# Optimization experiments

Measured on AMD Instinct MI355X. Metric: run time of the kernel, lower is better.

Reference implementation:

```python
import jax, jax.numpy as jnp
import numpy as np

N = 50000
E = 800000
D_IN = 128
D_OUT = 128
BN_EPS = 1e-5


def setup_inputs() -> dict:
    key = jax.random.key(0)
    ks = jax.random.split(key, 9)
    feature = jax.random.normal(ks[0], (N, D_IN), dtype=jnp.float32)
    snorm_n = jax.random.uniform(ks[1], (N, 1), dtype=jnp.float32)
    edge_src = jax.random.randint(ks[2], (E,), 0, N, dtype=jnp.int32)
    edge_dst = jax.random.randint(ks[3], (E,), 0, N, dtype=jnp.int32)
    # Linear(in,out,bias=False) weights, applied as x @ W (W stored [in,out])
    s = 1.0 / np.sqrt(D_IN)
    W1 = jax.random.uniform(ks[4], (D_IN, D_OUT), jnp.float32, -s, s)
    W2 = jax.random.uniform(ks[5], (D_IN, D_OUT), jnp.float32, -s, s)
    W3 = jax.random.uniform(ks[6], (D_IN, D_OUT), jnp.float32, -s, s)
    bias = jnp.zeros((D_OUT,), jnp.float32)
    gamma = jnp.ones((D_OUT,), jnp.float32)
    beta = jnp.zeros((D_OUT,), jnp.float32)
    return {"feature": feature, "snorm_n": snorm_n, "W1": W1, "W2": W2,
            "W3": W3, "bias": bias, "gamma": gamma, "beta": beta,
            "edge_src": edge_src, "edge_dst": edge_dst}


def _mpconv(feat, norm, edge_src, edge_dst):
    # feat: [N, D]; norm: [N, 1] = clamp(in_deg,1)^-0.5
    h = feat * norm
    msg = h[edge_src]                                   # gather [E, D]
    agg = jax.ops.segment_sum(msg, edge_dst, num_segments=N)  # scatter-add
    return agg * norm


def reference(feature, snorm_n, W1, W2, W3, bias, gamma, beta,
              edge_src, edge_dst):
    # in-degree normalization (same graph for both MP passes)
    deg = jax.ops.segment_sum(jnp.ones_like(edge_dst, jnp.float32),
                              edge_dst, num_segments=N)
    norm = jnp.power(jnp.clip(deg, 1.0, None), -0.5)[:, None]  # [N,1]

    h_in = feature
    ax = _mpconv(feature, norm, edge_src, edge_dst)
    ax2 = _mpconv(ax, norm, edge_src, edge_dst)

    h = (feature @ W1) + ((-ax) @ W2) + ((2.0 * ax2 - feature) @ W3) + bias
    h = h * snorm_n  # graph_norm

    # BatchNorm1d over nodes (training-mode batch statistics, biased var)
    mean = jnp.mean(h, axis=0)
    var = jnp.mean(jnp.square(h - mean), axis=0)
    h = (h - mean) * jax.lax.rsqrt(var + BN_EPS) * gamma + beta

    h = jax.nn.relu(h)      # activation
    h = h_in + h            # residual (in_dim == out_dim)
    # dropout p=0.0 -> identity
    return h
```

## Files before the change

kernel.cpp:

```cpp
#include <hip/hip_runtime.h>
#include <hip/hip_bf16.h>

#define NN 50000
#define NE 800000
#define DD 128
#define BN_EPS 1e-5f
#define SCAN_G 98

typedef unsigned short ushort_t;
typedef unsigned int uint_t;
typedef __attribute__((ext_vector_type(8))) short short8v;
typedef __attribute__((ext_vector_type(4))) float f32x4;

__device__ __forceinline__ float b2f(ushort_t u) {
    union { uint_t i; float f; } v; v.i = ((uint_t)u) << 16; return v.f;
}
__device__ __forceinline__ ushort_t f2b(float f) {
    uint_t u = __float_as_uint(f);
    u += 0x7FFFu + ((u >> 16) & 1u);
    return (ushort_t)(u >> 16);
}
__device__ __forceinline__ void atomAdd(float* p, float v) { unsafeAtomicAdd(p, v); }

__global__ void epos_kernel(const int* __restrict__ dst, int* __restrict__ cnt,
                            int* __restrict__ epos) {
    int e = blockIdx.x * 256 + threadIdx.x;
    if (e < NE) epos[e] = atomicAdd(&cnt[dst[e]], 1);
}

__global__ __launch_bounds__(512) void scan_part(const int* __restrict__ deg,
                                                 int* __restrict__ part,
                                                 float* __restrict__ norm) {
    int i = blockIdx.x * 512 + threadIdx.x;
    int v = (i < NN) ? deg[i] : 0;
    if (i < NN) norm[i] = rsqrtf((float)max(v, 1));
    int s = v;
    #pragma unroll
    for (int k = 1; k < 64; k <<= 1) s += __shfl_xor(s, k);
    __shared__ int wsum[8];
    if ((threadIdx.x & 63) == 0) wsum[threadIdx.x >> 6] = s;
    __syncthreads();
    if (threadIdx.x == 0) {
        int t = 0;
        #pragma unroll
        for (int k = 0; k < 8; ++k) t += wsum[k];
        part[blockIdx.x] = t;
    }
}

__global__ __launch_bounds__(512) void scan_final(const int* __restrict__ deg,
                                                  const int* __restrict__ part,
                                                  int* __restrict__ off) {
    __shared__ int wsum[8];
    __shared__ int sbase;
    int t = threadIdx.x;
    int lane = t & 63, wv = t >> 6;

    int p = (t < blockIdx.x && t < SCAN_G) ? part[t] : 0;
    #pragma unroll
    for (int s = 1; s < 64; s <<= 1) p += __shfl_xor(p, s);
    if (lane == 0) wsum[wv] = p;
    __syncthreads();
    if (t == 0) {
        int b = 0;
        #pragma unroll
        for (int k = 0; k < 8; ++k) b += wsum[k];
        sbase = b;
    }
    __syncthreads();

    int i = blockIdx.x * 512 + t;
    int v = (i < NN) ? deg[i] : 0;
    int incl = v;
    #pragma unroll
    for (int s = 1; s < 64; s <<= 1) {
        int u = __shfl_up(incl, s);
        if (lane >= s) incl += u;
    }
    __syncthreads();
    if (lane == 63) wsum[wv] = incl;
    __syncthreads();
    int woff = 0;
    for (int k = 0; k < wv; ++k) woff += wsum[k];
    int excl = sbase + woff + incl - v;
    if (i < NN) off[i] = excl;
    if (blockIdx.x == 0 && t == 0) off[NN] = NE;
}

__global__ void fill_kernel(const int* __restrict__ src, const int* __restrict__ dst,
                            const int* __restrict__ epos, const int* __restrict__ off,
                            const float* __restrict__ norm, int2* __restrict__ csr) {
    int e = blockIdx.x * 256 + threadIdx.x;
    if (e >= NE) return;
    int s = src[e];
    int p = off[dst[e]] + epos[e];
    csr[p] = make_int2(s, __float_as_int(norm[s]));
}

__global__ void prep_kernel(const float* __restrict__ feat, ushort_t* __restrict__ feat_bf,
                            const float* __restrict__ W1, const float* __restrict__ W2,
                            const float* __restrict__ W3, ushort_t* __restrict__ wcT) {
    int b = blockIdx.x;
    if (b < 6250) {
        int i = b * 256 + threadIdx.x;
        float4 v = reinterpret_cast<const float4*>(feat)[i];
        ushort4 o = { f2b(v.x), f2b(v.y), f2b(v.z), f2b(v.w) };
        reinterpret_cast<ushort4*>(feat_bf)[i] = o;
    } else {
        int i = (b - 6250) * 256 + threadIdx.x;
        if (i >= DD * 384) return;
        int d = i / 384, k = i % 384;
        float v;
        if (k < 128)      v = W1[k * DD + d] - W3[k * DD + d];
        else if (k < 256) v = -W2[(k - 128) * DD + d];
        else              v = 2.0f * W3[(k - 256) * DD + d];
        wcT[i] = f2b(v);
    }
}

__global__ __launch_bounds__(256) void gather_bf(const ushort_t* __restrict__ x,
                                                 const float* __restrict__ norm,
                                                 const int* __restrict__ off,
                                                 const int2* __restrict__ csr,
                                                 ushort_t* __restrict__ out) {
    int wid = (blockIdx.x << 2) + (threadIdx.x >> 6);
    int lane = threadIdx.x & 63;
    int q = lane >> 4, l4 = lane & 15;
    int jb = off[wid], je = off[wid + 1];
    const uint4* xp = reinterpret_cast<const uint4*>(x);
    float a0 = 0.f, a1 = 0.f, a2 = 0.f, a3 = 0.f;
    float a4 = 0.f, a5 = 0.f, a6 = 0.f, a7 = 0.f;

#define ACC(cc, vv)                                                  \
    {                                                                \
        float n_ = __int_as_float(cc.y);                             \
        a0 = fmaf(n_, b2f((ushort_t)vv.x), a0);                      \
        a1 = fmaf(n_, b2f((ushort_t)(vv.x >> 16)), a1);              \
        a2 = fmaf(n_, b2f((ushort_t)vv.y), a2);                      \
        a3 = fmaf(n_, b2f((ushort_t)(vv.y >> 16)), a3);              \
        a4 = fmaf(n_, b2f((ushort_t)vv.z), a4);                      \
        a5 = fmaf(n_, b2f((ushort_t)(vv.z >> 16)), a5);              \
        a6 = fmaf(n_, b2f((ushort_t)vv.w), a6);                      \
        a7 = fmaf(n_, b2f((ushort_t)(vv.w >> 16)), a7);              \
    }

    int j = jb;
    for (; j + 16 <= je; j += 16) {
        int2 c0 = csr[j + q];
        int2 c1 = csr[j + 4 + q];
        int2 c2 = csr[j + 8 + q];
        int2 c3 = csr[j + 12 + q];
        uint4 v0 = xp[(size_t)c0.x * 16 + l4];
        uint4 v1 = xp[(size_t)c1.x * 16 + l4];
        uint4 v2 = xp[(size_t)c2.x * 16 + l4];
        uint4 v3 = xp[(size_t)c3.x * 16 + l4];
        ACC(c0, v0); ACC(c1, v1); ACC(c2, v2); ACC(c3, v3);
    }
    for (; j < je; j += 4) {
        int jj = j + q;
        int2 c = (jj < je) ? csr[jj] : make_int2(0, 0);
        uint4 v = xp[(size_t)c.x * 16 + l4];
        ACC(c, v);
    }
#undef ACC

    a0 += __shfl_xor(a0, 16); a0 += __shfl_xor(a0, 32);
    a1 += __shfl_xor(a1, 16); a1 += __shfl_xor(a1, 32);
    a2 += __shfl_xor(a2, 16); a2 += __shfl_xor(a2, 32);
    a3 += __shfl_xor(a3, 16); a3 += __shfl_xor(a3, 32);
    a4 += __shfl_xor(a4, 16); a4 += __shfl_xor(a4, 32);
    a5 += __shfl_xor(a5, 16); a5 += __shfl_xor(a5, 32);
    a6 += __shfl_xor(a6, 16); a6 += __shfl_xor(a6, 32);
    a7 += __shfl_xor(a7, 16); a7 += __shfl_xor(a7, 32);
    if (q == 0) {
        float nd = norm[wid];
        uint4 o;
        o.x = (uint_t)f2b(nd * a0) | ((uint_t)f2b(nd * a1) << 16);
        o.y = (uint_t)f2b(nd * a2) | ((uint_t)f2b(nd * a3) << 16);
        o.z = (uint_t)f2b(nd * a4) | ((uint_t)f2b(nd * a5) << 16);
        o.w = (uint_t)f2b(nd * a6) | ((uint_t)f2b(nd * a7) << 16);
        reinterpret_cast<uint4*>(out)[(size_t)wid * 16 + l4] = o;
    }
}

__global__ __launch_bounds__(256) void gemm_bn(
    const ushort_t* __restrict__ feat_bf, const ushort_t* __restrict__ ax_bf,
    const ushort_t* __restrict__ ax2_bf, const ushort_t* __restrict__ wcT,
    const float* __restrict__ bias, const float* __restrict__ snorm,
    ushort_t* __restrict__ t_out, float* __restrict__ gsums, float* __restrict__ gsq)
{
    __shared__ ushort_t As[128 * 128];
    __shared__ ushort_t Bs[128 * 128];
    int tid = threadIdx.x;
    int w = tid >> 6, lane = tid & 63;
    int row0 = blockIdx.x * 128;

    f32x4 acc[2][8] = {};

    #pragma unroll
    for (int kt = 0; kt < 3; ++kt) {
        const ushort_t* S = (kt == 0) ? feat_bf : (kt == 1) ? ax_bf : ax2_bf;
        __syncthreads();
        {
            int r = tid >> 1, hh = tid & 1;
            int grow = min(row0 + r, NN - 1);
            const char* gsrc = (const char*)(S + grow * DD);
            char* dbase = (char*)As + r * 256;
            int sw = (r & 7) << 4;
            #pragma unroll
            for (int c = 0; c < 8; ++c) {
                int cb = hh * 128 + c * 16;
                *(short8v*)(dbase + (cb ^ sw)) = *(const short8v*)(gsrc + cb);
            }
        }
        {
            int cidx = tid >> 1, hh = tid & 1;
            const char* gsrc = (const char*)(wcT + cidx * 384 + kt * 128);
            char* dbase = (char*)Bs + cidx * 256;
            int sw = (cidx & 7) << 4;
            #pragma unroll
            for (int c = 0; c < 8; ++c) {
                int cb = hh * 128 + c * 16;
                *(short8v*)(dbase + (cb ^ sw)) = *(const short8v*)(gsrc + cb);
            }
        }
        __syncthreads();
        int l15 = lane & 15;
        int r0a = w * 32 + l15;
        int r1a = r0a + 16;
        #pragma unroll
        for (int ks = 0; ks < 4; ++ks) {
            int kb = ks * 64 + ((lane >> 4) << 4);
            short8v a0 = *(const short8v*)((const char*)As + r0a * 256 + (kb ^ ((r0a & 7) << 4)));
            short8v a1 = *(const short8v*)((const char*)As + r1a * 256 + (kb ^ ((r1a & 7) << 4)));
            #pragma unroll
            for (int cf = 0; cf < 8; ++cf) {
                int col = cf * 16 + l15;
                short8v b = *(const short8v*)((const char*)Bs + col * 256 + (kb ^ ((col & 7) << 4)));
                acc[0][cf] = __builtin_amdgcn_mfma_f32_16x16x32_bf16(a0, b, acc[0][cf], 0, 0, 0);
                acc[1][cf] = __builtin_amdgcn_mfma_f32_16x16x32_bf16(a1, b, acc[1][cf], 0, 0, 0);
            }
        }
    }

    int q = lane >> 4, c0 = lane & 15;
    float s1[8], s2[8];
    #pragma unroll
    for (int cf = 0; cf < 8; ++cf) { s1[cf] = 0.f; s2[cf] = 0.f; }

    #pragma unroll
    for (int g = 0; g < 2; ++g) {
        int rbase = row0 + w * 32 + g * 16 + q * 4;
        float sn[4];
        #pragma unroll
        for (int i = 0; i < 4; ++i) sn[i] = (rbase + i < NN) ? snorm[rbase + i] : 0.f;
        #pragma unroll
        for (int cf = 0; cf < 8; ++cf) {
            int col = cf * 16 + c0;
            float bc = bias[col];
            #pragma unroll
            for (int i = 0; i < 4; ++i) {
                int row = rbase + i;
                if (row < NN) {
                    float t = (acc[g][cf][i] + bc) * sn[i];
                    t_out[row * DD + col] = f2b(t);
                    s1[cf] += t; s2[cf] += t * t;
                }
            }
        }
    }
    #pragma unroll
    for (int cf = 0; cf < 8; ++cf) {
        s1[cf] += __shfl_xor(s1[cf], 16); s1[cf] += __shfl_xor(s1[cf], 32);
        s2[cf] += __shfl_xor(s2[cf], 16); s2[cf] += __shfl_xor(s2[cf], 32);
    }
    if (q == 0) {
        int slot = (blockIdx.x & 31) * DD;
        #pragma unroll
        for (int cf = 0; cf < 8; ++cf) {
            atomAdd(&gsums[slot + cf * 16 + c0], s1[cf]);
            atomAdd(&gsq[slot + cf * 16 + c0], s2[cf]);
        }
    }
}

__global__ void bn_finalize(const float* __restrict__ gsums, const float* __restrict__ gsq,
                            const float* __restrict__ gamma,
                            const float* __restrict__ beta,
                            float* __restrict__ scale, float* __restrict__ shift) {
    int d = threadIdx.x;
    float s1 = 0.f, s2 = 0.f;
    for (int c = 0; c < 32; ++c) { s1 += gsums[c * DD + d]; s2 += gsq[c * DD + d]; }
    float mean = s1 / (float)NN;
    float var  = s2 / (float)NN - mean * mean;
    float sc = gamma[d] * rsqrtf(var + BN_EPS);
    scale[d] = sc;
    shift[d] = beta[d] - mean * sc;
}

__global__ void epilogue(const ushort_t* __restrict__ t, const ushort_t* __restrict__ featb,
                         const float* __restrict__ scale, const float* __restrict__ shift,
                         float* __restrict__ out) {
    int i = blockIdx.x * 256 + threadIdx.x;
    if (i >= NN * DD / 4) return;
    int d0 = (i << 2) & 127;
    ushort4 tv = reinterpret_cast<const ushort4*>(t)[i];
    ushort4 fv = reinterpret_cast<const ushort4*>(featb)[i];
    float4 o;
    o.x = b2f(fv.x) + fmaxf(b2f(tv.x) * scale[d0 + 0] + shift[d0 + 0], 0.f);
    o.y = b2f(fv.y) + fmaxf(b2f(tv.y) * scale[d0 + 1] + shift[d0 + 1], 0.f);
    o.z = b2f(fv.z) + fmaxf(b2f(tv.z) * scale[d0 + 2] + shift[d0 + 2], 0.f);
    o.w = b2f(fv.w) + fmaxf(b2f(tv.w) * scale[d0 + 3] + shift[d0 + 3], 0.f);
    reinterpret_cast<float4*>(out)[i] = o;
}

extern "C" void kernel_launch(void* const* d_in, const int* in_sizes, int n_in,
                              void* d_out, int out_size, void* d_ws, size_t ws_size,
                              hipStream_t stream) {
    const float* feat  = (const float*)d_in[0];
    const float* snorm = (const float*)d_in[1];
    const float* W1    = (const float*)d_in[2];
    const float* W2    = (const float*)d_in[3];
    const float* W3    = (const float*)d_in[4];
    const float* bias  = (const float*)d_in[5];
    const float* gamma = (const float*)d_in[6];
    const float* beta  = (const float*)d_in[7];
    const int* esrc = (const int*)d_in[8];
    const int* edst = (const int*)d_in[9];
    float* out = (float*)d_out;

    char* ws = (char*)d_ws;
    ushort_t* t_bf    = (ushort_t*)(ws);
    int*      epos    = (int*)     (ws);
    ushort_t* feat_bf = (ushort_t*)(ws + 12800000);
    ushort_t* ax_bf   = (ushort_t*)(ws + 25600000);
    ushort_t* ax2_bf  = (ushort_t*)(ws + 38400000);
    int2*     csr     = (int2*)    (ws + 51200000);
    float*    norm    = (float*)   (ws + 57600000);
    int*      cnt     = (int*)     (ws + 57800000);
    float*    gsums   = (float*)   (ws + 58000000);
    float*    gsq     = (float*)   (ws + 58016384);
    int*      off     = (int*)     (ws + 58032768);
    int*      part    = (int*)     (ws + 58232832);
    float*    scale   = (float*)   (ws + 58233856);
    float*    shift   = (float*)   (ws + 58234368);
    ushort_t* wcT     = (ushort_t*)(ws + 58234880);

    hipMemsetAsync(ws + 57800000, 0, 232768, stream);

    epos_kernel<<<3125, 256, 0, stream>>>(edst, cnt, epos);
    scan_part  <<<SCAN_G, 512, 0, stream>>>(cnt, part, norm);
    scan_final <<<SCAN_G, 512, 0, stream>>>(cnt, part, off);
    fill_kernel<<<3125, 256, 0, stream>>>(esrc, edst, epos, off, norm, csr);

    prep_kernel<<<6442, 256, 0, stream>>>(feat, feat_bf, W1, W2, W3, wcT);

    gather_bf<<<12500, 256, 0, stream>>>(feat_bf, norm, off, csr, ax_bf);
    gather_bf<<<12500, 256, 0, stream>>>(ax_bf,   norm, off, csr, ax2_bf);

    gemm_bn<<<391, 256, 0, stream>>>(feat_bf, ax_bf, ax2_bf, wcT, bias, snorm,
                                     t_bf, gsums, gsq);
    bn_finalize<<<1, 128, 0, stream>>>(gsums, gsq, gamma, beta, scale, shift);
    epilogue   <<<6250, 256, 0, stream>>>(t_bf, feat_bf, scale, shift, out);
}
```

Baseline: 175.6 us.

## Map one 16-lane group per node in gather and fold prep into setup kernels

The gather kernel now gives each destination node a 16-lane group instead of a full 64-lane wavefront. Each lane loops over that node's edges serially, which removes the cross-lane shuffle reduction and the idle-quarter masking, and the kernel launches with a quarter as many blocks. The feature bf16 conversion moves into the epos kernel and the weight combine into extra blocks of scan_final, which drops the separate prep launch. The trade-off is fewer edge loads in flight per node and more divergence between the four nodes that share a wavefront when their degrees differ.

```diff
diff --git a/kernel.cpp b/kernel.cpp
--- a/kernel.cpp
+++ b/kernel.cpp
@@ -22,10 +22,20 @@
 }
 __device__ __forceinline__ void atomAdd(float* p, float v) { unsafeAtomicAdd(p, v); }
 
-__global__ void epos_kernel(const int* __restrict__ dst, int* __restrict__ cnt,
-                            int* __restrict__ epos) {
+__global__ void epos_prep(const int* __restrict__ dst, int* __restrict__ cnt,
+                          int* __restrict__ epos,
+                          const float* __restrict__ feat, ushort_t* __restrict__ feat_bf) {
     int e = blockIdx.x * 256 + threadIdx.x;
-    if (e < NE) epos[e] = atomicAdd(&cnt[dst[e]], 1);
+    {
+        const float4* fp = reinterpret_cast<const float4*>(feat);
+        ushort4* op = reinterpret_cast<ushort4*>(feat_bf);
+        int i = e << 1;
+        float4 v0 = fp[i], v1 = fp[i + 1];
+        ushort4 o0 = { f2b(v0.x), f2b(v0.y), f2b(v0.z), f2b(v0.w) };
+        ushort4 o1 = { f2b(v1.x), f2b(v1.y), f2b(v1.z), f2b(v1.w) };
+        op[i] = o0; op[i + 1] = o1;
+    }
+    epos[e] = atomicAdd(&cnt[dst[e]], 1);
 }
 
 __global__ __launch_bounds__(512) void scan_part(const int* __restrict__ deg,
@@ -50,7 +60,21 @@
 
 __global__ __launch_bounds__(512) void scan_final(const int* __restrict__ deg,
                                                   const int* __restrict__ part,
-                                                  int* __restrict__ off) {
+                                                  int* __restrict__ off,
+                                                  const float* __restrict__ W1,
+                                                  const float* __restrict__ W2,
+                                                  const float* __restrict__ W3,
+                                                  ushort_t* __restrict__ wcT) {
+    if (blockIdx.x >= SCAN_G) {
+        int i = (blockIdx.x - SCAN_G) * 512 + threadIdx.x;
+        int d = i / 384, k = i % 384;
+        float v;
+        if (k < 128)      v = W1[k * DD + d] - W3[k * DD + d];
+        else if (k < 256) v = -W2[(k - 128) * DD + d];
+        else              v = 2.0f * W3[(k - 256) * DD + d];
+        wcT[i] = f2b(v);
+        return;
+    }
     __shared__ int wsum[8];
     __shared__ int sbase;
     int t = threadIdx.x;
@@ -97,36 +121,14 @@
     csr[p] = make_int2(s, __float_as_int(norm[s]));
 }
 
-__global__ void prep_kernel(const float* __restrict__ feat, ushort_t* __restrict__ feat_bf,
-                            const float* __restrict__ W1, const float* __restrict__ W2,
-                            const float* __restrict__ W3, ushort_t* __restrict__ wcT) {
-    int b = blockIdx.x;
-    if (b < 6250) {
-        int i = b * 256 + threadIdx.x;
-        float4 v = reinterpret_cast<const float4*>(feat)[i];
-        ushort4 o = { f2b(v.x), f2b(v.y), f2b(v.z), f2b(v.w) };
-        reinterpret_cast<ushort4*>(feat_bf)[i] = o;
-    } else {
-        int i = (b - 6250) * 256 + threadIdx.x;
-        if (i >= DD * 384) return;
-        int d = i / 384, k = i % 384;
-        float v;
-        if (k < 128)      v = W1[k * DD + d] - W3[k * DD + d];
-        else if (k < 256) v = -W2[(k - 128) * DD + d];
-        else              v = 2.0f * W3[(k - 256) * DD + d];
-        wcT[i] = f2b(v);
-    }
-}
-
 __global__ __launch_bounds__(256) void gather_bf(const ushort_t* __restrict__ x,
                                                  const float* __restrict__ norm,
                                                  const int* __restrict__ off,
                                                  const int2* __restrict__ csr,
                                                  ushort_t* __restrict__ out) {
-    int wid = (blockIdx.x << 2) + (threadIdx.x >> 6);
-    int lane = threadIdx.x & 63;
-    int q = lane >> 4, l4 = lane & 15;
-    int jb = off[wid], je = off[wid + 1];
+    int g = (blockIdx.x << 4) | (threadIdx.x >> 4);
+    int l4 = threadIdx.x & 15;
+    int jb = off[g], je = off[g + 1];
     const uint4* xp = reinterpret_cast<const uint4*>(x);
     float a0 = 0.f, a1 = 0.f, a2 = 0.f, a3 = 0.f;
     float a4 = 0.f, a5 = 0.f, a6 = 0.f, a7 = 0.f;
@@ -134,53 +136,42 @@
 #define ACC(cc, vv)                                                  \
     {                                                                \
         float n_ = __int_as_float(cc.y);                             \
-        a0 = fmaf(n_, b2f((ushort_t)vv.x), a0);                      \
+        a0 = fmaf(n_, b2f((ushort_t)(vv.x)), a0);                    \
         a1 = fmaf(n_, b2f((ushort_t)(vv.x >> 16)), a1);              \
-        a2 = fmaf(n_, b2f((ushort_t)vv.y), a2);                      \
+        a2 = fmaf(n_, b2f((ushort_t)(vv.y)), a2);                    \
         a3 = fmaf(n_, b2f((ushort_t)(vv.y >> 16)), a3);              \
-        a4 = fmaf(n_, b2f((ushort_t)vv.z), a4);                      \
+        a4 = fmaf(n_, b2f((ushort_t)(vv.z)), a4);                    \
         a5 = fmaf(n_, b2f((ushort_t)(vv.z >> 16)), a5);              \
-        a6 = fmaf(n_, b2f((ushort_t)vv.w), a6);                      \
+        a6 = fmaf(n_, b2f((ushort_t)(vv.w)), a6);                    \
         a7 = fmaf(n_, b2f((ushort_t)(vv.w >> 16)), a7);              \
     }
 
     int j = jb;
-    for (; j + 16 <= je; j += 16) {
-        int2 c0 = csr[j + q];
-        int2 c1 = csr[j + 4 + q];
-        int2 c2 = csr[j + 8 + q];
-        int2 c3 = csr[j + 12 + q];
+    for (; j + 4 <= je; j += 4) {
+        int2 c0 = csr[j + 0];
+        int2 c1 = csr[j + 1];
+        int2 c2 = csr[j + 2];
+        int2 c3 = csr[j + 3];
         uint4 v0 = xp[(size_t)c0.x * 16 + l4];
         uint4 v1 = xp[(size_t)c1.x * 16 + l4];
         uint4 v2 = xp[(size_t)c2.x * 16 + l4];
         uint4 v3 = xp[(size_t)c3.x * 16 + l4];
         ACC(c0, v0); ACC(c1, v1); ACC(c2, v2); ACC(c3, v3);
     }
-    for (; j < je; j += 4) {
-        int jj = j + q;
-        int2 c = (jj < je) ? csr[jj] : make_int2(0, 0);
+    for (; j < je; ++j) {
+        int2 c = csr[j];
         uint4 v = xp[(size_t)c.x * 16 + l4];
         ACC(c, v);
     }
 #undef ACC
 
-    a0 += __shfl_xor(a0, 16); a0 += __shfl_xor(a0, 32);
-    a1 += __shfl_xor(a1, 16); a1 += __shfl_xor(a1, 32);
-    a2 += __shfl_xor(a2, 16); a2 += __shfl_xor(a2, 32);
-    a3 += __shfl_xor(a3, 16); a3 += __shfl_xor(a3, 32);
-    a4 += __shfl_xor(a4, 16); a4 += __shfl_xor(a4, 32);
-    a5 += __shfl_xor(a5, 16); a5 += __shfl_xor(a5, 32);
-    a6 += __shfl_xor(a6, 16); a6 += __shfl_xor(a6, 32);
-    a7 += __shfl_xor(a7, 16); a7 += __shfl_xor(a7, 32);
-    if (q == 0) {
-        float nd = norm[wid];
-        uint4 o;
-        o.x = (uint_t)f2b(nd * a0) | ((uint_t)f2b(nd * a1) << 16);
-        o.y = (uint_t)f2b(nd * a2) | ((uint_t)f2b(nd * a3) << 16);
-        o.z = (uint_t)f2b(nd * a4) | ((uint_t)f2b(nd * a5) << 16);
-        o.w = (uint_t)f2b(nd * a6) | ((uint_t)f2b(nd * a7) << 16);
-        reinterpret_cast<uint4*>(out)[(size_t)wid * 16 + l4] = o;
-    }
+    float nd = norm[g];
+    uint4 o;
+    o.x = (uint_t)f2b(nd * a0) | ((uint_t)f2b(nd * a1) << 16);
+    o.y = (uint_t)f2b(nd * a2) | ((uint_t)f2b(nd * a3) << 16);
+    o.z = (uint_t)f2b(nd * a4) | ((uint_t)f2b(nd * a5) << 16);
+    o.w = (uint_t)f2b(nd * a6) | ((uint_t)f2b(nd * a7) << 16);
+    reinterpret_cast<uint4*>(out)[(size_t)g * 16 + l4] = o;
 }
 
 __global__ __launch_bounds__(256) void gemm_bn(
@@ -348,15 +339,13 @@
 
     hipMemsetAsync(ws + 57800000, 0, 232768, stream);
 
-    epos_kernel<<<3125, 256, 0, stream>>>(edst, cnt, epos);
+    epos_prep  <<<3125, 256, 0, stream>>>(edst, cnt, epos, feat, feat_bf);
     scan_part  <<<SCAN_G, 512, 0, stream>>>(cnt, part, norm);
-    scan_final <<<SCAN_G, 512, 0, stream>>>(cnt, part, off);
+    scan_final <<<SCAN_G + 96, 512, 0, stream>>>(cnt, part, off, W1, W2, W3, wcT);
     fill_kernel<<<3125, 256, 0, stream>>>(esrc, edst, epos, off, norm, csr);
 
-    prep_kernel<<<6442, 256, 0, stream>>>(feat, feat_bf, W1, W2, W3, wcT);
-
-    gather_bf<<<12500, 256, 0, stream>>>(feat_bf, norm, off, csr, ax_bf);
-    gather_bf<<<12500, 256, 0, stream>>>(ax_bf,   norm, off, csr, ax2_bf);
+    gather_bf<<<3125, 256, 0, stream>>>(feat_bf, norm, off, csr, ax_bf);
+    gather_bf<<<3125, 256, 0, stream>>>(ax_bf,   norm, off, csr, ax2_bf);
 
     gemm_bn<<<391, 256, 0, stream>>>(feat_bf, ax_bf, ax2_bf, wcT, bias, snorm,
                                      t_bf, gsums, gsq);
```

Result: faster. 166.8 us (-5.0%).
